# Optimization experiments

Hardware: AMD Instinct MI355X
Metric: run time of the kernel (lower is better)

## Reference

```python
import jax, jax.numpy as jnp
import numpy as np

B, S, D, H = 4, 2048, 1024, 16
HD = D // H
FF = 4 * D
EPS = 1e-5


def setup_inputs() -> dict:
    key = jax.random.key(0)
    ks = jax.random.split(key, 12)
    s = lambda fan_in: 1.0 / np.sqrt(fan_in)
    inp = {
        "x": jax.random.normal(ks[0], (B, S, D), dtype=jnp.float32),
        # attention weights stored as (d_in, d_out)
        "Wq": jax.random.normal(ks[1], (D, D), dtype=jnp.float32) * s(D),
        "Wk": jax.random.normal(ks[2], (D, D), dtype=jnp.float32) * s(D),
        "Wv": jax.random.normal(ks[3], (D, D), dtype=jnp.float32) * s(D),
        "Wo": jax.random.normal(ks[4], (D, D), dtype=jnp.float32) * s(D),
        "bo": jnp.zeros((D,), dtype=jnp.float32),
        # feed-forward
        "W1": jax.random.normal(ks[5], (D, FF), dtype=jnp.float32) * s(D),
        "b1": jnp.zeros((FF,), dtype=jnp.float32),
        "W2": jax.random.normal(ks[6], (FF, D), dtype=jnp.float32) * s(FF),
        "b2": jnp.zeros((D,), dtype=jnp.float32),
        # layernorms
        "g1": jnp.ones((D,), dtype=jnp.float32),
        "be1": jnp.zeros((D,), dtype=jnp.float32),
        "g2": jnp.ones((D,), dtype=jnp.float32),
        "be2": jnp.zeros((D,), dtype=jnp.float32),
    }
    return inp


def _layernorm(x, gamma, beta):
    mean = jnp.mean(x, axis=-1, keepdims=True)
    var = jnp.mean(jnp.square(x - mean), axis=-1, keepdims=True)  # unbiased=False
    return gamma * (x - mean) / jnp.sqrt(var + EPS) + beta


def _gelu_tanh(x):
    c = jnp.sqrt(jnp.asarray(2.0 / jnp.pi, dtype=x.dtype))
    return 0.5 * x * (1.0 + jnp.tanh(c * (x + 0.044715 * x * x * x)))


def _block(x, Wq, Wk, Wv, Wo, bo, W1, b1, W2, b2, g1, be1, g2, be2):
    # --- pre-LN causal multi-head attention ---
    shortcut = x
    h = _layernorm(x, g1, be1)
    q = (h @ Wq).reshape(B, S, H, HD).transpose(0, 2, 1, 3)  # [B,H,S,HD]
    k = (h @ Wk).reshape(B, S, H, HD).transpose(0, 2, 1, 3)
    v = (h @ Wv).reshape(B, S, H, HD).transpose(0, 2, 1, 3)
    scores = jnp.einsum("bhqd,bhkd->bhqk", q, k)
    causal = jnp.tril(jnp.ones((S, S), dtype=bool))  # True = keep
    scores = jnp.where(causal, scores, -jnp.inf)
    attn = jax.nn.softmax(scores / jnp.sqrt(jnp.asarray(HD, scores.dtype)), axis=-1)
    ctx = jnp.einsum("bhqk,bhkd->bqhd", attn, v).reshape(B, S, D)
    x = ctx @ Wo + bo + shortcut
    # --- pre-LN GELU MLP ---
    shortcut = x
    h = _layernorm(x, g2, be2)
    h = _gelu_tanh(h @ W1 + b1) @ W2 + b2
    return h + shortcut


def reference(x, Wq, Wk, Wv, Wo, bo, W1, b1, W2, b2, g1, be1, g2, be2):
    return _block(x, Wq, Wk, Wv, Wo, bo, W1, b1, W2, b2, g1, be1, g2, be2)
```

## Files before the change

kernel.cpp:

```cpp
#include <hip/hip_runtime.h>
#include <cstdint>

#define B_   4
#define S_   2048
#define D_   1024
#define H_   16
#define HD_  64
#define FF_  4096
#define MTOK 8192

typedef short s16x8 __attribute__((ext_vector_type(8), may_alias));
typedef float f32x4 __attribute__((ext_vector_type(4)));
typedef unsigned short u16x4 __attribute__((ext_vector_type(4), may_alias));
typedef unsigned short u16x8 __attribute__((ext_vector_type(8), may_alias));

#define GLD_LDS16(g, l)                                                  \
  __builtin_amdgcn_global_load_lds(                                      \
      (__attribute__((address_space(1))) void*)(g),                      \
      (__attribute__((address_space(3))) void*)(l), 16, 0, 0)

__device__ __forceinline__ unsigned short f2bf(float f) {
  unsigned u = __float_as_uint(f);
  unsigned r = 0x7fffu + ((u >> 16) & 1u);
  return (unsigned short)((u + r) >> 16);
}

__global__ __launch_bounds__(256) void k_transpose(const float* __restrict__ in,
                                                   unsigned short* __restrict__ out,
                                                   int R, int C) {
  __shared__ float tile[32][33];
  int tx = threadIdx.x, ty = threadIdx.y;
  int c0 = blockIdx.x * 32, r0 = blockIdx.y * 32;
#pragma unroll
  for (int j = 0; j < 4; ++j)
    tile[ty + j * 8][tx] = in[(size_t)(r0 + ty + j * 8) * C + (c0 + tx)];
  __syncthreads();
#pragma unroll
  for (int j = 0; j < 4; ++j)
    out[(size_t)(c0 + ty + j * 8) * R + (r0 + tx)] = f2bf(tile[tx][ty + j * 8]);
}

__global__ __launch_bounds__(256) void k_layernorm(const float* __restrict__ x,
                                                   const float* __restrict__ g,
                                                   const float* __restrict__ be,
                                                   unsigned short* __restrict__ out) {
  int row = blockIdx.x, t = threadIdx.x;
  const float4* xr = (const float4*)(x + (size_t)row * D_);
  float4 v = xr[t];
  float s = v.x + v.y + v.z + v.w;
  float q = v.x * v.x + v.y * v.y + v.z * v.z + v.w * v.w;
#pragma unroll
  for (int o = 1; o < 64; o <<= 1) { s += __shfl_xor(s, o); q += __shfl_xor(q, o); }
  __shared__ float red[8];
  int wid = t >> 6;
  if ((t & 63) == 0) { red[wid * 2] = s; red[wid * 2 + 1] = q; }
  __syncthreads();
  s = red[0] + red[2] + red[4] + red[6];
  q = red[1] + red[3] + red[5] + red[7];
  float mean = s * (1.0f / D_);
  float rstd = rsqrtf(q * (1.0f / D_) - mean * mean + 1e-5f);
  float4 gv = ((const float4*)g)[t];
  float4 bv = ((const float4*)be)[t];
  u16x4 o4;
  o4[0] = f2bf(gv.x * (v.x - mean) * rstd + bv.x);
  o4[1] = f2bf(gv.y * (v.y - mean) * rstd + bv.y);
  o4[2] = f2bf(gv.z * (v.z - mean) * rstd + bv.z);
  o4[3] = f2bf(gv.w * (v.w - mean) * rstd + bv.w);
  *(u16x4*)(out + (size_t)row * D_ + t * 4) = o4;
}

template <int MODE>
__global__ __launch_bounds__(512, 2) void k_gemmdp(
    const unsigned short* __restrict__ A, const unsigned short* __restrict__ Bt,
    const float* __restrict__ bias, const float* __restrict__ resid,
    unsigned short* __restrict__ outb, float* __restrict__ outf,
    int M, int N, int K) {
  constexpr int BM = 128, BN = 256, BK = 64;
  constexpr int AE = BM * BK;
  constexpr int BE = BN * BK;
  constexpr int BUF_E = AE + BE;
  __shared__ __align__(16) unsigned short smem[3 * BUF_E];
  unsigned short* const Rs = smem;

  const int tid = threadIdx.x;
  const int wid = tid >> 6, lane = tid & 63;
  const int l16 = lane & 15, lg = lane >> 4;
  const int wr = wid >> 2, wc = wid & 3;
  const int nwg = gridDim.x * gridDim.y;
  const int id = blockIdx.y * gridDim.x + blockIdx.x;
  const int swz = (id & 7) * (nwg >> 3) + (id >> 3);
  const int m0 = (swz / gridDim.x) * BM, n0 = (swz % gridDim.x) * BN;

  f32x4 acc[4][4];
#pragma unroll
  for (int m = 0; m < 4; ++m)
#pragma unroll
    for (int n = 0; n < 4; ++n) acc[m][n] = (f32x4)0.0f;

  const unsigned short* aSrc[2]; int aDstB[2];
  const unsigned short* bSrc[4]; int bDstB[4];
#pragma unroll
  for (int g = 0; g < 2; ++g) {
    int q = g * 512 + tid, row = q >> 3, c = q & 7;
    aSrc[g] = A + (size_t)(m0 + row) * K + ((c ^ (row & 7)) << 3);
    aDstB[g] = q * 16;
  }
#pragma unroll
  for (int g = 0; g < 4; ++g) {
    int q = g * 512 + tid, row = q >> 3, c = q & 7;
    bSrc[g] = Bt + (size_t)(n0 + row) * K + ((c ^ (row & 7)) << 3);
    bDstB[g] = q * 16;
  }
  int cSw[2];
  cSw[0] = ((lg) ^ (l16 & 7)) * 8;
  cSw[1] = ((4 + lg) ^ (l16 & 7)) * 8;
  const int aRow = (wr * 64 + l16) * BK;
  const int bRow = (wc * 64 + l16) * BK;

#define STAGE(ti)                                                              \
  {                                                                            \
    const int _b = (ti) % 3;                                                   \
    char* _pa = (char*)(smem + _b * BUF_E);                                    \
    char* _pb = (char*)(smem + _b * BUF_E + AE);                               \
    const int _kt = (ti) * BK;                                                 \
    _Pragma("unroll")                                                          \
    for (int g = 0; g < 2; ++g) GLD_LDS16(aSrc[g] + _kt, _pa + aDstB[g]);      \
    _Pragma("unroll")                                                          \
    for (int g = 0; g < 4; ++g) GLD_LDS16(bSrc[g] + _kt, _pb + bDstB[g]);      \
  }

  const int nt = K / BK;
  STAGE(0); STAGE(1);
  asm volatile("s_waitcnt vmcnt(6)" ::: "memory");
  __builtin_amdgcn_sched_barrier(0);
  __builtin_amdgcn_s_barrier();

  for (int i = 0; i < nt; ++i) {
    if (i + 2 < nt) STAGE(i + 2);
    const unsigned short* pa = smem + (i % 3) * BUF_E + aRow;
    const unsigned short* pb = smem + (i % 3) * BUF_E + AE + bRow;
    s16x8 af[4][2], bfr[4][2];
#pragma unroll
    for (int m = 0; m < 4; ++m) {
      af[m][0] = *(const s16x8*)(pa + m * 16 * BK + cSw[0]);
      af[m][1] = *(const s16x8*)(pa + m * 16 * BK + cSw[1]);
    }
#pragma unroll
    for (int n = 0; n < 4; ++n) {
      bfr[n][0] = *(const s16x8*)(pb + n * 16 * BK + cSw[0]);
      bfr[n][1] = *(const s16x8*)(pb + n * 16 * BK + cSw[1]);
    }
    asm volatile("s_waitcnt lgkmcnt(0)" ::: "memory");
    __builtin_amdgcn_sched_barrier(0);
    __builtin_amdgcn_s_setprio(1);
#pragma unroll
    for (int m = 0; m < 4; ++m)
#pragma unroll
      for (int n = 0; n < 4; ++n) {
        acc[m][n] = __builtin_amdgcn_mfma_f32_16x16x32_bf16(af[m][0], bfr[n][0], acc[m][n], 0, 0, 0);
        acc[m][n] = __builtin_amdgcn_mfma_f32_16x16x32_bf16(af[m][1], bfr[n][1], acc[m][n], 0, 0, 0);
      }
    __builtin_amdgcn_s_setprio(0);
    if (i < nt - 2) {
      asm volatile("s_waitcnt vmcnt(6)" ::: "memory");
    } else if (i == nt - 2) {
      asm volatile("s_waitcnt vmcnt(0)" ::: "memory");
    }
    __builtin_amdgcn_sched_barrier(0);
    __builtin_amdgcn_s_barrier();
  }
#undef STAGE

  if constexpr (MODE == 2) {
#pragma unroll
    for (int n = 0; n < 4; ++n) {
      const int col = n0 + wc * 64 + n * 16 + l16;
      const float bv = bias[col];
#pragma unroll
      for (int m = 0; m < 4; ++m)
#pragma unroll
        for (int r = 0; r < 4; ++r) {
          const int row = m0 + wr * 64 + m * 16 + lg * 4 + r;
          outf[(size_t)row * N + col] = acc[m][n][r] + bv + resid[(size_t)row * N + col];
        }
    }
    return;
  }

#define ROWMAJOR_FLUSH(DSTPTR, NSTRIDE, COLBASE, XFORM)                        \
  {                                                                            \
    _Pragma("unroll")                                                          \
    for (int p = 0; p < 2; ++p) {                                              \
      if (wr == p) {                                                           \
        _Pragma("unroll")                                                      \
        for (int n = 0; n < 4; ++n) {                                          \
          _Pragma("unroll")                                                    \
          for (int mm = 0; mm < 4; ++mm) {                                     \
            _Pragma("unroll")                                                  \
            for (int r = 0; r < 4; ++r) {                                      \
              float xv = acc[mm][n][r];                                        \
              XFORM;                                                           \
              Rs[(mm * 16 + lg * 4 + r) * 264 + wc * 64 + n * 16 + l16] = f2bf(xv); \
            }                                                                  \
          }                                                                    \
        }                                                                      \
      }                                                                        \
      __syncthreads();                                                         \
      const int row_l = tid >> 3;                                              \
      _Pragma("unroll")                                                        \
      for (int j = 0; j < 4; ++j) {                                            \
        const int c = (tid & 7) * 4 + j;                                       \
        u16x8 vv = *(const u16x8*)(Rs + row_l * 264 + c * 8);                  \
        *(u16x8*)((DSTPTR) + (size_t)(m0 + p * 64 + row_l) * (NSTRIDE) +       \
                  (COLBASE) + c * 8) = vv;                                     \
      }                                                                        \
      if (p == 0) __syncthreads();                                             \
    }                                                                          \
  }

  if constexpr (MODE == 1) {
    ROWMAJOR_FLUSH(outb, N, n0, {
      xv += bias[n0 + wc * 64 + n * 16 + l16];
      float uu = 0.7978845608028654f * (xv + 0.044715f * xv * xv * xv);
      xv = xv * __builtin_amdgcn_rcpf(1.0f + __builtin_amdgcn_exp2f(uu * -2.885390081777927f));
    });
    return;
  }

  if constexpr (MODE == 3) {
    unsigned short* qout = outb;
    unsigned short* kout = outb + (size_t)MTOK * D_;
    unsigned short* vout = outb + 2 * (size_t)MTOK * D_;
    if (n0 < 1024) {
      ROWMAJOR_FLUSH(qout, D_, n0, { xv *= 0.125f; });
    } else if (n0 < 2048) {
      ROWMAJOR_FLUSH(kout, D_, n0 - 1024, {});
    } else {
      const int vbase = (m0 >> 11) * 1024 + (n0 - 2048);
      const int srow0 = m0 & 2047;
#pragma unroll
      for (int g = 0; g < 4; ++g) {
        if (wc == g) {
#pragma unroll
          for (int n = 0; n < 4; ++n)
#pragma unroll
            for (int m = 0; m < 4; ++m) {
              u16x4 pk;
#pragma unroll
              for (int r = 0; r < 4; ++r) pk[r] = f2bf(acc[m][n][r]);
              *(u16x4*)(Rs + (n * 16 + l16) * 264 + wr * 64 + m * 16 + lg * 4) = pk;
            }
        }
        __syncthreads();
        const int row_l = tid >> 3;
#pragma unroll
        for (int j = 0; j < 2; ++j) {
          const int c = (tid & 7) * 2 + j;
          u16x8 vv = *(const u16x8*)(Rs + row_l * 264 + c * 8);
          *(u16x8*)(vout + (size_t)(vbase + g * 64 + row_l) * S_ + srow0 + c * 8) = vv;
        }
        if (g < 3) __syncthreads();
      }
    }
    return;
  }
#undef ROWMAJOR_FLUSH
}

__global__ __launch_bounds__(256, 3) void k_attn(
    const unsigned short* __restrict__ qg, const unsigned short* __restrict__ kg,
    const unsigned short* __restrict__ vtg, unsigned short* __restrict__ ctx) {
  const int id = blockIdx.x;
  const int bh = (id & 7) + 8 * (id >> 7);
  const int p  = (id >> 3) & 15;
  const int qtA = p, qtB = 31 - p;
  const int tid = threadIdx.x, wid = tid >> 6, lane = tid & 63;
  const int l16 = lane & 15, lg = lane >> 4;
  __shared__ __align__(16) unsigned short Ks[2][64 * 64];
  __shared__ __align__(16) unsigned short Vs[2][64 * 64];
  __shared__ __align__(16) unsigned short Ps[4][2][16 * 72];

  const size_t headoff = (size_t)(bh >> 4) * ((size_t)S_ * D_) + (size_t)(bh & 15) * HD_;
  const unsigned short* Kb = kg + headoff;
  const unsigned short* Vt = vtg + (size_t)bh * ((size_t)HD_ * S_);

  const int qrowA = qtA * 64 + wid * 16 + l16;
  const int qrowB = qtB * 64 + wid * 16 + l16;
  s16x8 qfA0 = *(const s16x8*)(qg + headoff + (size_t)qrowA * D_ + lg * 8);
  s16x8 qfA1 = *(const s16x8*)(qg + headoff + (size_t)qrowA * D_ + 32 + lg * 8);
  s16x8 qfB0 = *(const s16x8*)(qg + headoff + (size_t)qrowB * D_ + lg * 8);
  s16x8 qfB1 = *(const s16x8*)(qg + headoff + (size_t)qrowB * D_ + 32 + lg * 8);

  f32x4 oA[4], oB[4];
#pragma unroll
  for (int n = 0; n < 4; ++n) { oA[n] = (f32x4)0.0f; oB[n] = (f32x4)0.0f; }
  float lsumA[4] = {0.f, 0.f, 0.f, 0.f};
  float lsumB[4] = {0.f, 0.f, 0.f, 0.f};
  unsigned short* psA = &Ps[wid][0][0];
  unsigned short* psB = &Ps[wid][1][0];
  const int myrowA = qtA * 64 + wid * 16 + lg * 4;
  const int myrowB = qtB * 64 + wid * 16 + lg * 4;
  const float L2E = 1.4426950408889634f;

  const unsigned short* kSrc[2];
  const unsigned short* vSrc[2];
  int dstOff[2];
#pragma unroll
  for (int i = 0; i < 2; ++i) {
    int chunk = (i * 4 + wid) * 64 + lane;
    int row = chunk >> 3, pc = chunk & 7;
    int scol = (pc ^ (row & 7)) * 8;
    kSrc[i] = Kb + (size_t)row * D_ + scol;
    vSrc[i] = Vt + (size_t)row * S_ + scol;
    dstOff[i] = (i * 4 + wid) * 1024;
  }

#pragma unroll
  for (int i = 0; i < 2; ++i) {
    GLD_LDS16(kSrc[i], (char*)Ks[0] + dstOff[i]);
    GLD_LDS16(vSrc[i], (char*)Vs[0] + dstOff[i]);
  }
  __syncthreads();

  for (int t = 0; t <= qtB; ++t) {
    const int cur = t & 1;
    const int kv0 = t * 64;
    const bool doA = (t <= qtA);
    if (t < qtB) {
      const int kvn = kv0 + 64;
#pragma unroll
      for (int i = 0; i < 2; ++i) {
        GLD_LDS16(kSrc[i] + (size_t)kvn * D_, (char*)Ks[cur ^ 1] + dstOff[i]);
        GLD_LDS16(vSrc[i] + kvn, (char*)Vs[cur ^ 1] + dstOff[i]);
      }
    }
    const unsigned short* Kc = Ks[cur];
    const unsigned short* Vc = Vs[cur];
    s16x8 kf0[4], kf1[4];
#pragma unroll
    for (int n = 0; n < 4; ++n) {
      int srow = n * 16 + l16, sw = srow & 7;
      kf0[n] = *(const s16x8*)(Kc + srow * 64 + (lg ^ sw) * 8);
      kf1[n] = *(const s16x8*)(Kc + srow * 64 + ((4 + lg) ^ sw) * 8);
    }
    f32x4 saA[4], saB[4];
    if (doA) {
#pragma unroll
      for (int n = 0; n < 4; ++n) {
        saA[n] = (f32x4)0.0f;
        saA[n] = __builtin_amdgcn_mfma_f32_16x16x32_bf16(qfA0, kf0[n], saA[n], 0, 0, 0);
        saA[n] = __builtin_amdgcn_mfma_f32_16x16x32_bf16(qfA1, kf1[n], saA[n], 0, 0, 0);
      }
    }
#pragma unroll
    for (int n = 0; n < 4; ++n) {
      saB[n] = (f32x4)0.0f;
      saB[n] = __builtin_amdgcn_mfma_f32_16x16x32_bf16(qfB0, kf0[n], saB[n], 0, 0, 0);
      saB[n] = __builtin_amdgcn_mfma_f32_16x16x32_bf16(qfB1, kf1[n], saB[n], 0, 0, 0);
    }
    if (doA) {
      const bool mask = (t == qtA);
#pragma unroll
      for (int r = 0; r < 4; ++r)
#pragma unroll
        for (int n = 0; n < 4; ++n) {
          float pv = exp2f((saA[n][r] - 12.0f) * L2E);
          if (mask && (kv0 + n * 16 + l16) > (myrowA + r)) pv = 0.0f;
          lsumA[r] += pv;
          psA[(lg * 4 + r) * 72 + n * 16 + l16] = f2bf(pv);
        }
    }
    {
      const bool mask = (t == qtB);
#pragma unroll
      for (int r = 0; r < 4; ++r)
#pragma unroll
        for (int n = 0; n < 4; ++n) {
          float pv = exp2f((saB[n][r] - 12.0f) * L2E);
          if (mask && (kv0 + n * 16 + l16) > (myrowB + r)) pv = 0.0f;
          lsumB[r] += pv;
          psB[(lg * 4 + r) * 72 + n * 16 + l16] = f2bf(pv);
        }
    }
    s16x8 vf0[4], vf1[4];
#pragma unroll
    for (int n = 0; n < 4; ++n) {
      int srow = n * 16 + l16, sw = srow & 7;
      vf0[n] = *(const s16x8*)(Vc + srow * 64 + (lg ^ sw) * 8);
      vf1[n] = *(const s16x8*)(Vc + srow * 64 + ((4 + lg) ^ sw) * 8);
    }
    __builtin_amdgcn_sched_barrier(0);
    asm volatile("s_waitcnt lgkmcnt(0)" ::: "memory");
    __builtin_amdgcn_sched_barrier(0);
    {
      s16x8 paB0 = *(const s16x8*)(psB + l16 * 72 + lg * 8);
      s16x8 paB1 = *(const s16x8*)(psB + l16 * 72 + 32 + lg * 8);
#pragma unroll
      for (int n = 0; n < 4; ++n) {
        oB[n] = __builtin_amdgcn_mfma_f32_16x16x32_bf16(paB0, vf0[n], oB[n], 0, 0, 0);
        oB[n] = __builtin_amdgcn_mfma_f32_16x16x32_bf16(paB1, vf1[n], oB[n], 0, 0, 0);
      }
      if (doA) {
        s16x8 paA0 = *(const s16x8*)(psA + l16 * 72 + lg * 8);
        s16x8 paA1 = *(const s16x8*)(psA + l16 * 72 + 32 + lg * 8);
#pragma unroll
        for (int n = 0; n < 4; ++n) {
          oA[n] = __builtin_amdgcn_mfma_f32_16x16x32_bf16(paA0, vf0[n], oA[n], 0, 0, 0);
          oA[n] = __builtin_amdgcn_mfma_f32_16x16x32_bf16(paA1, vf1[n], oA[n], 0, 0, 0);
        }
      }
    }
    __syncthreads();
  }

#pragma unroll
  for (int r = 0; r < 4; ++r) {
    float la = lsumA[r], lb = lsumB[r];
    la += __shfl_xor(la, 1); lb += __shfl_xor(lb, 1);
    la += __shfl_xor(la, 2); lb += __shfl_xor(lb, 2);
    la += __shfl_xor(la, 4); lb += __shfl_xor(lb, 4);
    la += __shfl_xor(la, 8); lb += __shfl_xor(lb, 8);
    float ia = 1.0f / la, ib = 1.0f / lb;
#pragma unroll
    for (int n = 0; n < 4; ++n) {
      ctx[headoff + (size_t)(myrowA + r) * D_ + n * 16 + l16] = f2bf(oA[n][r] * ia);
      ctx[headoff + (size_t)(myrowB + r) * D_ + n * 16 + l16] = f2bf(oB[n][r] * ib);
    }
  }
}

extern "C" void kernel_launch(void* const* d_in, const int* in_sizes, int n_in,
                              void* d_out, int out_size, void* d_ws, size_t ws_size,
                              hipStream_t stream) {
  (void)in_sizes; (void)n_in; (void)out_size; (void)ws_size;
  const float* x   = (const float*)d_in[0];
  const float* Wq  = (const float*)d_in[1];
  const float* Wk  = (const float*)d_in[2];
  const float* Wv  = (const float*)d_in[3];
  const float* Wo  = (const float*)d_in[4];
  const float* bo  = (const float*)d_in[5];
  const float* W1  = (const float*)d_in[6];
  const float* b1  = (const float*)d_in[7];
  const float* W2  = (const float*)d_in[8];
  const float* b2  = (const float*)d_in[9];
  const float* g1  = (const float*)d_in[10];
  const float* be1 = (const float*)d_in[11];
  const float* g2  = (const float*)d_in[12];
  const float* be2 = (const float*)d_in[13];
  float* out = (float*)d_out;

  char* w = (char*)d_ws;
  const size_t MB = 1ull << 20;
  unsigned short* wqkvT = (unsigned short*)(w + 0 * MB);
  unsigned short* woT   = (unsigned short*)(w + 6 * MB);
  unsigned short* w1T   = (unsigned short*)(w + 8 * MB);
  unsigned short* w2T   = (unsigned short*)(w + 16 * MB);
  unsigned short* hb    = (unsigned short*)(w + 24 * MB);
  float*          x2    = (float*)(w + 40 * MB);
  unsigned short* qkv   = (unsigned short*)(w + 72 * MB);
  unsigned short* qb    = qkv;
  unsigned short* kb    = qkv + (size_t)MTOK * D_;
  unsigned short* vbT   = qkv + 2 * (size_t)MTOK * D_;
  unsigned short* cxb   = (unsigned short*)(w + 120 * MB);
  unsigned short* act   = (unsigned short*)(w + 72 * MB);

  dim3 tb(32, 8);
  k_transpose<<<dim3(32, 32), tb, 0, stream>>>(Wq, wqkvT, 1024, 1024);
  k_transpose<<<dim3(32, 32), tb, 0, stream>>>(Wk, wqkvT + 1024 * 1024, 1024, 1024);
  k_transpose<<<dim3(32, 32), tb, 0, stream>>>(Wv, wqkvT + 2048 * 1024, 1024, 1024);
  k_transpose<<<dim3(32, 32), tb, 0, stream>>>(Wo, woT, 1024, 1024);
  k_transpose<<<dim3(128, 32), tb, 0, stream>>>(W1, w1T, 1024, 4096);
  k_transpose<<<dim3(32, 128), tb, 0, stream>>>(W2, w2T, 4096, 1024);

  k_layernorm<<<MTOK, 256, 0, stream>>>(x, g1, be1, hb);

  k_gemmdp<3><<<dim3(12, 64), 512, 0, stream>>>(hb, wqkvT, nullptr, nullptr, qkv, nullptr, MTOK, 3072, 1024);

  k_attn<<<1024, 256, 0, stream>>>(qb, kb, vbT, cxb);

  k_gemmdp<2><<<dim3(4, 64), 512, 0, stream>>>(cxb, woT, bo, x, nullptr, x2, MTOK, 1024, 1024);

  k_layernorm<<<MTOK, 256, 0, stream>>>(x2, g2, be2, hb);

  k_gemmdp<1><<<dim3(16, 64), 512, 0, stream>>>(hb, w1T, b1, nullptr, act, nullptr, MTOK, 4096, 1024);
  k_gemmdp<2><<<dim3(4, 64), 512, 0, stream>>>(act, w2T, b2, x2, nullptr, out, MTOK, 1024, 4096);
}
```

Measured before the change: 430.3 us.

## Add 256x256-tile GEMM with 8-phase pipelined staging for QKV and FFN1

Adds a new GEMM kernel with 256x256 output tiles and a 64-wide K step. Loads are split into four 64-row quarter-tiles that are double-buffered in LDS, and each load is interleaved with a matching MFMA phase under setprio and XOR-swizzled LDS addressing. The kernel replaces the 128x256 kernel for the QKV projection and the first FFN GEMM, aiming for more operand reuse per LDS byte and better overlap of global loads with MFMA. The cost is a larger LDS footprint (128 KB) and 128 accumulator registers per thread, which may limit occupancy. The grids also halve, giving 384 and 512 workgroups.

```diff
diff --git a/kernel.cpp b/kernel.cpp
--- a/kernel.cpp
+++ b/kernel.cpp
@@ -70,6 +70,209 @@
 }
 
 template <int MODE>
+__global__ __launch_bounds__(512, 2) void k_gemm8p(
+    const unsigned short* __restrict__ A, const unsigned short* __restrict__ Bt,
+    const float* __restrict__ bias,
+    unsigned short* __restrict__ outb,
+    int M, int N, int K) {
+  __shared__ __align__(16) unsigned short smem[8 * 8192];
+  unsigned short* const Rs = smem;
+
+  const int tid = threadIdx.x;
+  const int wid = tid >> 6, lane = tid & 63;
+  const int l16 = lane & 15, lg = lane >> 4;
+  const int wr = wid >> 2, wc = wid & 3;
+  const int nwg = gridDim.x * gridDim.y;
+  const int id = blockIdx.y * gridDim.x + blockIdx.x;
+  const int swz = (id & 7) * (nwg >> 3) + (id >> 3);
+  const int m0 = (swz / gridDim.x) * 256, n0 = (swz % gridDim.x) * 256;
+
+  f32x4 acc[8][4];
+#pragma unroll
+  for (int m = 0; m < 8; ++m)
+#pragma unroll
+    for (int n = 0; n < 4; ++n) acc[m][n] = (f32x4)0.0f;
+
+  const int sRow = tid >> 3;
+  const int sC = (((tid & 7) ^ (sRow & 7)) << 3);
+  const unsigned short* aS0 = A + (size_t)(m0 + sRow) * K + sC;
+  const unsigned short* aS1 = A + (size_t)(m0 + 64 + sRow) * K + sC;
+  const unsigned short* aS2 = A + (size_t)(m0 + 128 + sRow) * K + sC;
+  const unsigned short* aS3 = A + (size_t)(m0 + 192 + sRow) * K + sC;
+  const unsigned short* bS0 = Bt + (size_t)(n0 + sRow) * K + sC;
+  const unsigned short* bS1 = Bt + (size_t)(n0 + 64 + sRow) * K + sC;
+  const unsigned short* bS2 = Bt + (size_t)(n0 + 128 + sRow) * K + sC;
+  const unsigned short* bS3 = Bt + (size_t)(n0 + 192 + sRow) * K + sC;
+  const int d0 = tid * 16, d1 = tid * 16 + 8192;
+
+  const int cS0 = ((lg ^ (l16 & 7)) << 3);
+  const int cS1 = (((4 + lg) ^ (l16 & 7)) << 3);
+
+  const int nt = K / 64;
+
+  GLD_LDS16(aS0, (char*)(smem + 0 * 8192) + d0);
+  GLD_LDS16(aS1, (char*)(smem + 0 * 8192) + d1);
+  GLD_LDS16(bS0, (char*)(smem + 1 * 8192) + d0);
+  GLD_LDS16(bS1, (char*)(smem + 1 * 8192) + d1);
+  GLD_LDS16(bS2, (char*)(smem + 2 * 8192) + d0);
+  GLD_LDS16(bS3, (char*)(smem + 2 * 8192) + d1);
+  GLD_LDS16(aS2, (char*)(smem + 3 * 8192) + d0);
+  GLD_LDS16(aS3, (char*)(smem + 3 * 8192) + d1);
+  asm volatile("s_waitcnt vmcnt(4)" ::: "memory");
+  __builtin_amdgcn_sched_barrier(0);
+  __builtin_amdgcn_s_barrier();
+
+#define PHASE(P, WSTR, DOSTAGE)                                                \
+  {                                                                            \
+    constexpr int mq_ = (P) >> 1, nh_ = (P) & 1;                               \
+    const unsigned short* Au = smem + ((kt & 1) * 4 + (mq_ ? 3 : 0)) * 8192;   \
+    const unsigned short* Bu = smem + ((kt & 1) * 4 + 1 + nh_) * 8192;         \
+    s16x8 af[4][2], bf[2][2];                                                  \
+    _Pragma("unroll")                                                          \
+    for (int m4 = 0; m4 < 4; ++m4) {                                           \
+      const unsigned short* pr_ = Au + (wr * 64 + m4 * 16 + l16) * 64;         \
+      af[m4][0] = *(const s16x8*)(pr_ + cS0);                                  \
+      af[m4][1] = *(const s16x8*)(pr_ + cS1);                                  \
+    }                                                                          \
+    _Pragma("unroll")                                                          \
+    for (int n2 = 0; n2 < 2; ++n2) {                                           \
+      const unsigned short* pr_ = Bu + (wc * 32 + n2 * 16 + l16) * 64;         \
+      bf[n2][0] = *(const s16x8*)(pr_ + cS0);                                  \
+      bf[n2][1] = *(const s16x8*)(pr_ + cS1);                                  \
+    }                                                                          \
+    if (DOSTAGE) {                                                             \
+      char* dst_ = (char*)(smem + (((kt + 1) & 1) * 4 + (P)) * 8192);          \
+      const size_t ko_ = (size_t)(kt + 1) * 64;                                \
+      if constexpr ((P) == 0) {                                                \
+        GLD_LDS16(aS0 + ko_, dst_ + d0); GLD_LDS16(aS1 + ko_, dst_ + d1);      \
+      } else if constexpr ((P) == 1) {                                         \
+        GLD_LDS16(bS0 + ko_, dst_ + d0); GLD_LDS16(bS1 + ko_, dst_ + d1);      \
+      } else if constexpr ((P) == 2) {                                         \
+        GLD_LDS16(bS2 + ko_, dst_ + d0); GLD_LDS16(bS3 + ko_, dst_ + d1);      \
+      } else {                                                                 \
+        GLD_LDS16(aS2 + ko_, dst_ + d0); GLD_LDS16(aS3 + ko_, dst_ + d1);      \
+      }                                                                        \
+    }                                                                          \
+    asm volatile("s_waitcnt lgkmcnt(0)" ::: "memory");                         \
+    __builtin_amdgcn_sched_barrier(0);                                         \
+    __builtin_amdgcn_s_setprio(1);                                             \
+    _Pragma("unroll")                                                          \
+    for (int m4 = 0; m4 < 4; ++m4)                                             \
+      _Pragma("unroll")                                                        \
+      for (int n2 = 0; n2 < 2; ++n2) {                                         \
+        acc[mq_ * 4 + m4][nh_ * 2 + n2] = __builtin_amdgcn_mfma_f32_16x16x32_bf16( \
+            af[m4][0], bf[n2][0], acc[mq_ * 4 + m4][nh_ * 2 + n2], 0, 0, 0);   \
+        acc[mq_ * 4 + m4][nh_ * 2 + n2] = __builtin_amdgcn_mfma_f32_16x16x32_bf16( \
+            af[m4][1], bf[n2][1], acc[mq_ * 4 + m4][nh_ * 2 + n2], 0, 0, 0);   \
+      }                                                                        \
+    __builtin_amdgcn_s_setprio(0);                                             \
+    asm volatile("s_waitcnt vmcnt(" WSTR ")" ::: "memory");                    \
+    __builtin_amdgcn_sched_barrier(0);                                         \
+    __builtin_amdgcn_s_barrier();                                              \
+  }
+
+  for (int kt = 0; kt < nt - 1; ++kt) {
+    PHASE(0, "4", true)
+    PHASE(1, "4", true)
+    PHASE(2, "4", true)
+    PHASE(3, "4", true)
+  }
+  {
+    const int kt = nt - 1;
+    PHASE(0, "2", false)
+    PHASE(1, "0", false)
+    PHASE(2, "0", false)
+    PHASE(3, "0", false)
+  }
+#undef PHASE
+
+#define RM_FLUSH8(DSTPTR, NSTRIDE, COLBASE, XFORM)                             \
+  {                                                                            \
+    _Pragma("unroll")                                                          \
+    for (int pr = 0; pr < 4; ++pr) {                                           \
+      if (wr == (pr & 1)) {                                                    \
+        const int mb_ = (pr >> 1) * 4;                                         \
+        _Pragma("unroll")                                                      \
+        for (int nn = 0; nn < 4; ++nn) {                                       \
+          const int col = (nn >> 1) * 128 + wc * 32 + (nn & 1) * 16 + l16;     \
+          _Pragma("unroll")                                                    \
+          for (int m4 = 0; m4 < 4; ++m4) {                                     \
+            _Pragma("unroll")                                                  \
+            for (int r = 0; r < 4; ++r) {                                      \
+              float xv = acc[mb_ + m4][nn][r];                                 \
+              XFORM;                                                           \
+              Rs[(m4 * 16 + lg * 4 + r) * 264 + col] = f2bf(xv);               \
+            }                                                                  \
+          }                                                                    \
+        }                                                                      \
+      }                                                                        \
+      __syncthreads();                                                         \
+      const int row_l = tid >> 3;                                              \
+      _Pragma("unroll")                                                        \
+      for (int j = 0; j < 4; ++j) {                                            \
+        const int c = (tid & 7) * 4 + j;                                       \
+        u16x8 vv = *(const u16x8*)(Rs + row_l * 264 + c * 8);                  \
+        *(u16x8*)((DSTPTR) + (size_t)(m0 + pr * 64 + row_l) * (NSTRIDE) +      \
+                  (COLBASE) + c * 8) = vv;                                     \
+      }                                                                        \
+      if (pr < 3) __syncthreads();                                             \
+    }                                                                          \
+  }
+
+  if constexpr (MODE == 1) {
+    RM_FLUSH8(outb, N, n0, {
+      xv += bias[n0 + col];
+      float uu = 0.7978845608028654f * (xv + 0.044715f * xv * xv * xv);
+      xv = xv * __builtin_amdgcn_rcpf(1.0f + __builtin_amdgcn_exp2f(uu * -2.885390081777927f));
+    });
+    return;
+  }
+
+  if constexpr (MODE == 3) {
+    unsigned short* qout = outb;
+    unsigned short* kout = outb + (size_t)MTOK * D_;
+    unsigned short* vout = outb + 2 * (size_t)MTOK * D_;
+    if (n0 < 1024) {
+      RM_FLUSH8(qout, D_, n0, { xv *= 0.125f; });
+    } else if (n0 < 2048) {
+      RM_FLUSH8(kout, D_, n0 - 1024, {});
+    } else {
+      const int vbase = (m0 >> 11) * 1024 + (n0 - 2048);
+      const int srow0 = m0 & 2047;
+#pragma unroll
+      for (int cg = 0; cg < 4; ++cg) {
+        if ((wc >> 1) == (cg & 1)) {
+          const int nhh = (cg >> 1) * 2;
+#pragma unroll
+          for (int n2 = 0; n2 < 2; ++n2) {
+            const int colL = (wc & 1) * 32 + n2 * 16 + l16;
+#pragma unroll
+            for (int m = 0; m < 8; ++m) {
+              const int rowL = (m >> 2) * 128 + wr * 64 + (m & 3) * 16 + lg * 4;
+              u16x4 pk;
+#pragma unroll
+              for (int r = 0; r < 4; ++r) pk[r] = f2bf(acc[m][nhh + n2][r]);
+              *(u16x4*)(Rs + colL * 264 + rowL) = pk;
+            }
+          }
+        }
+        __syncthreads();
+        const int colf = tid >> 3;
+#pragma unroll
+        for (int j = 0; j < 4; ++j) {
+          u16x8 vv = *(const u16x8*)(Rs + colf * 264 + (tid & 7) * 32 + j * 8);
+          *(u16x8*)(vout + (size_t)(vbase + cg * 64 + colf) * S_ + srow0 +
+                    (tid & 7) * 32 + j * 8) = vv;
+        }
+        if (cg < 3) __syncthreads();
+      }
+    }
+    return;
+  }
+#undef RM_FLUSH8
+}
+
+template <int MODE>
 __global__ __launch_bounds__(512, 2) void k_gemmdp(
     const unsigned short* __restrict__ A, const unsigned short* __restrict__ Bt,
     const float* __restrict__ bias, const float* __restrict__ resid,
@@ -80,7 +283,6 @@
   constexpr int BE = BN * BK;
   constexpr int BUF_E = AE + BE;
   __shared__ __align__(16) unsigned short smem[3 * BUF_E];
-  unsigned short* const Rs = smem;
 
   const int tid = threadIdx.x;
   const int wid = tid >> 6, lane = tid & 63;
@@ -184,87 +386,8 @@
           outf[(size_t)row * N + col] = acc[m][n][r] + bv + resid[(size_t)row * N + col];
         }
     }
-    return;
-  }
-
-#define ROWMAJOR_FLUSH(DSTPTR, NSTRIDE, COLBASE, XFORM)                        \
-  {                                                                            \
-    _Pragma("unroll")                                                          \
-    for (int p = 0; p < 2; ++p) {                                              \
-      if (wr == p) {                                                           \
-        _Pragma("unroll")                                                      \
-        for (int n = 0; n < 4; ++n) {                                          \
-          _Pragma("unroll")                                                    \
-          for (int mm = 0; mm < 4; ++mm) {                                     \
-            _Pragma("unroll")                                                  \
-            for (int r = 0; r < 4; ++r) {                                      \
-              float xv = acc[mm][n][r];                                        \
-              XFORM;                                                           \
-              Rs[(mm * 16 + lg * 4 + r) * 264 + wc * 64 + n * 16 + l16] = f2bf(xv); \
-            }                                                                  \
-          }                                                                    \
-        }                                                                      \
-      }                                                                        \
-      __syncthreads();                                                         \
-      const int row_l = tid >> 3;                                              \
-      _Pragma("unroll")                                                        \
-      for (int j = 0; j < 4; ++j) {                                            \
-        const int c = (tid & 7) * 4 + j;                                       \
-        u16x8 vv = *(const u16x8*)(Rs + row_l * 264 + c * 8);                  \
-        *(u16x8*)((DSTPTR) + (size_t)(m0 + p * 64 + row_l) * (NSTRIDE) +       \
-                  (COLBASE) + c * 8) = vv;                                     \
-      }                                                                        \
-      if (p == 0) __syncthreads();                                             \
-    }                                                                          \
-  }
-
-  if constexpr (MODE == 1) {
-    ROWMAJOR_FLUSH(outb, N, n0, {
-      xv += bias[n0 + wc * 64 + n * 16 + l16];
-      float uu = 0.7978845608028654f * (xv + 0.044715f * xv * xv * xv);
-      xv = xv * __builtin_amdgcn_rcpf(1.0f + __builtin_amdgcn_exp2f(uu * -2.885390081777927f));
-    });
-    return;
-  }
-
-  if constexpr (MODE == 3) {
-    unsigned short* qout = outb;
-    unsigned short* kout = outb + (size_t)MTOK * D_;
-    unsigned short* vout = outb + 2 * (size_t)MTOK * D_;
-    if (n0 < 1024) {
-      ROWMAJOR_FLUSH(qout, D_, n0, { xv *= 0.125f; });
-    } else if (n0 < 2048) {
-      ROWMAJOR_FLUSH(kout, D_, n0 - 1024, {});
-    } else {
-      const int vbase = (m0 >> 11) * 1024 + (n0 - 2048);
-      const int srow0 = m0 & 2047;
-#pragma unroll
-      for (int g = 0; g < 4; ++g) {
-        if (wc == g) {
-#pragma unroll
-          for (int n = 0; n < 4; ++n)
-#pragma unroll
-            for (int m = 0; m < 4; ++m) {
-              u16x4 pk;
-#pragma unroll
-              for (int r = 0; r < 4; ++r) pk[r] = f2bf(acc[m][n][r]);
-              *(u16x4*)(Rs + (n * 16 + l16) * 264 + wr * 64 + m * 16 + lg * 4) = pk;
-            }
-        }
-        __syncthreads();
-        const int row_l = tid >> 3;
-#pragma unroll
-        for (int j = 0; j < 2; ++j) {
-          const int c = (tid & 7) * 2 + j;
-          u16x8 vv = *(const u16x8*)(Rs + row_l * 264 + c * 8);
-          *(u16x8*)(vout + (size_t)(vbase + g * 64 + row_l) * S_ + srow0 + c * 8) = vv;
-        }
-        if (g < 3) __syncthreads();
-      }
-    }
-    return;
-  }
-#undef ROWMAJOR_FLUSH
+  }
+  (void)outb;
 }
 
 __global__ __launch_bounds__(256, 3) void k_attn(
@@ -474,7 +597,7 @@
 
   k_layernorm<<<MTOK, 256, 0, stream>>>(x, g1, be1, hb);
 
-  k_gemmdp<3><<<dim3(12, 64), 512, 0, stream>>>(hb, wqkvT, nullptr, nullptr, qkv, nullptr, MTOK, 3072, 1024);
+  k_gemm8p<3><<<dim3(12, 32), 512, 0, stream>>>(hb, wqkvT, nullptr, qkv, MTOK, 3072, 1024);
 
   k_attn<<<1024, 256, 0, stream>>>(qb, kb, vbT, cxb);
 
@@ -482,6 +605,6 @@
 
   k_layernorm<<<MTOK, 256, 0, stream>>>(x2, g2, be2, hb);
 
-  k_gemmdp<1><<<dim3(16, 64), 512, 0, stream>>>(hb, w1T, b1, nullptr, act, nullptr, MTOK, 4096, 1024);
+  k_gemm8p<1><<<dim3(16, 32), 512, 0, stream>>>(hb, w1T, b1, act, MTOK, 4096, 1024);
   k_gemmdp<2><<<dim3(4, 64), 512, 0, stream>>>(act, w2T, b2, x2, nullptr, out, MTOK, 1024, 4096);
 }
```

After: 423.1 us. Within noise of the previous version (-1.7%).
